# Performance work log

Hardware: AMD Instinct MI355X
Metric: run time of the kernel (lower is better)

The kernel has to match this reference:

```python
import jax, jax.numpy as jnp
import numpy as np
from jax import lax

VOCAB = 50000
EMB = 10
HID = 16


def setup_inputs() -> dict:
    key = jax.random.key(0)
    ks = jax.random.split(key, 8)
    B, T = 4096, 512
    x = jax.random.randint(ks[0], (B, T), 0, VOCAB + 1)
    emb = jax.random.normal(ks[1], (VOCAB + 1, EMB), dtype=jnp.float32)
    emb = emb.at[0].set(0.0)  # padding_idx=0 row is zeros
    s_ih = 1.0 / np.sqrt(HID)
    Wih = jax.random.uniform(ks[2], (4 * HID, EMB), minval=-s_ih, maxval=s_ih, dtype=jnp.float32)
    Whh = jax.random.uniform(ks[3], (4 * HID, HID), minval=-s_ih, maxval=s_ih, dtype=jnp.float32)
    bih = jax.random.uniform(ks[4], (4 * HID,), minval=-s_ih, maxval=s_ih, dtype=jnp.float32)
    bhh = jax.random.uniform(ks[5], (4 * HID,), minval=-s_ih, maxval=s_ih, dtype=jnp.float32)
    Wfc = jax.random.uniform(ks[6], (1, HID), minval=-s_ih, maxval=s_ih, dtype=jnp.float32)
    bfc = jax.random.uniform(ks[7], (1,), minval=-s_ih, maxval=s_ih, dtype=jnp.float32)
    return {"x": x, "emb": emb, "Wih": Wih, "Whh": Whh, "bih": bih, "bhh": bhh, "Wfc": Wfc, "bfc": bfc}


def _lstm_last_h(xe, Wih, Whh, bih, bhh):
    # xe: [B, T, EMB] -> final hidden state [B, HID]. PyTorch gate order: i, f, g, o.
    B = xe.shape[0]
    h0 = jnp.zeros((B, HID), dtype=xe.dtype)
    c0 = jnp.zeros((B, HID), dtype=xe.dtype)
    # Precompute input projections for all timesteps: [T, B, 4H]
    xproj = jnp.einsum('btе,ge->btg'.replace('\u0435', 'e'), xe, Wih) + bih + bhh
    xproj = xproj.transpose(1, 0, 2)

    def step(carry, xp_t):
        h, c = carry
        gates = xp_t + h @ Whh.T  # [B, 4H]
        i, f, g, o = jnp.split(gates, 4, axis=-1)
        i = jax.nn.sigmoid(i)
        f = jax.nn.sigmoid(f)
        g = jnp.tanh(g)
        o = jax.nn.sigmoid(o)
        c = f * c + i * g
        h = o * jnp.tanh(c)
        return (h, c), None

    (h, _), _ = lax.scan(step, (h0, c0), xproj)
    return h


def reference(x, emb, Wih, Whh, bih, bhh, Wfc, bfc):
    xe = emb[x]  # [B, T, EMB] embedding lookup (padding row 0 is zero)
    h = _lstm_last_h(xe, Wih, Whh, bih, bhh)  # [B, HID]
    out = h @ Wfc.T + bfc  # [B, 1]
    return jax.nn.sigmoid(out)
```

## Files before the change

kernel.cpp:

```cpp
#include <hip/hip_runtime.h>

#define T_LEN 512
#define NHID 16
#define NEMB 10
#define VOCAB1 50001
#define IROW 520

typedef float v2f __attribute__((ext_vector_type(2)));

__global__ __launch_bounds__(256) void build_table(
    const float* __restrict__ emb, const float* __restrict__ Wih,
    const float* __restrict__ bih, const float* __restrict__ bhh,
    float* __restrict__ tbl)
{
    const int tid = blockIdx.x * 256 + threadIdx.x;
    if (tid >= VOCAB1 * 16) return;
    const int v = tid >> 4, j = tid & 15;
    float e[NEMB];
    #pragma unroll
    for (int i = 0; i < NEMB; ++i) e[i] = emb[v * NEMB + i];
    float o[4];
    #pragma unroll
    for (int q = 0; q < 4; ++q) {
        const int r = q * 16 + j;
        float a = bih[r] + bhh[r];
        #pragma unroll
        for (int i = 0; i < NEMB; ++i) a += e[i] * Wih[r * NEMB + i];
        o[q] = a;
    }
    ((float4*)tbl)[tid] = make_float4(o[0], o[1], o[2], o[3]);
}

#define DPP_ROR(dst, src_i, r)                                                   \
    dst = __builtin_bit_cast(float, __builtin_amdgcn_update_dpp(                 \
              0, src_i, 0x120 + r, 0xF, 0xF, true))

__global__ __launch_bounds__(256) void lstm_dpp_kernel(
    const int*   __restrict__ x,
    const float* __restrict__ tbl,
    const float* __restrict__ Whh,
    const float* __restrict__ Wfc,
    const float* __restrict__ bfc,
    float*       __restrict__ out)
{
    __shared__ int idxs[16][IROW];

    const int tid = threadIdx.x;
    const int j   = tid & 15;
    const int lb  = tid >> 4;
    const int batch = blockIdx.x * 16 + lb;

    #pragma unroll 1
    for (int b = 0; b < 16; ++b) {
        const int* xr = x + (size_t)(blockIdx.x * 16 + b) * T_LEN;
        for (int t = tid; t < IROW; t += 256)
            idxs[b][t] = (t < T_LEN) ? (xr[t] << 4) : 0;
    }
    __syncthreads();

    float w[4][16];
    #pragma unroll
    for (int q = 0; q < 4; ++q) {
        const int row = (q * 16 + j) * NHID;
        #pragma unroll
        for (int r = 0; r < 16; ++r)
            w[q][r] = Whh[row + ((j - r) & 15)];
    }

    float h = 0.f, c = 0.f;
    const float NL2E  = -1.44269504088896f;
    const float NL2E2 = -2.88539008177793f;
    const float4* t4 = (const float4*)tbl;

    float4 pf[4];
    #pragma unroll
    for (int s = 0; s < 4; ++s)
        pf[s] = t4[idxs[lb][s] + j];

    #pragma unroll 1
    for (int t = 0; t < T_LEN; t += 4) {
        #pragma unroll
        for (int u = 0; u < 4; ++u) {
            const float4 tb = pf[u];
            pf[u] = t4[idxs[lb][t + 4 + u] + j];

            float hr[16];
            const int hvi = __builtin_bit_cast(int, h);
            hr[0] = h;
            DPP_ROR(hr[1],  hvi, 1);   DPP_ROR(hr[2],  hvi, 2);
            DPP_ROR(hr[3],  hvi, 3);   DPP_ROR(hr[4],  hvi, 4);
            DPP_ROR(hr[5],  hvi, 5);   DPP_ROR(hr[6],  hvi, 6);
            DPP_ROR(hr[7],  hvi, 7);   DPP_ROR(hr[8],  hvi, 8);
            DPP_ROR(hr[9],  hvi, 9);   DPP_ROR(hr[10], hvi, 10);
            DPP_ROR(hr[11], hvi, 11);  DPP_ROR(hr[12], hvi, 12);
            DPP_ROR(hr[13], hvi, 13);  DPP_ROR(hr[14], hvi, 14);
            DPP_ROR(hr[15], hvi, 15);

            float a0 = tb.x, a1 = tb.y, a2 = tb.z, a3 = tb.w;
            #pragma unroll
            for (int r = 0; r < 16; ++r) {
                a0 = fmaf(hr[r], w[0][r], a0);
                a1 = fmaf(hr[r], w[1][r], a1);
                a2 = fmaf(hr[r], w[2][r], a2);
                a3 = fmaf(hr[r], w[3][r], a3);
            }

            const float ig = __builtin_amdgcn_rcpf(1.f + __builtin_amdgcn_exp2f(a0 * NL2E));
            const float fg = __builtin_amdgcn_rcpf(1.f + __builtin_amdgcn_exp2f(a1 * NL2E));
            const float gg = 2.f * __builtin_amdgcn_rcpf(1.f + __builtin_amdgcn_exp2f(a2 * NL2E2)) - 1.f;
            const float og = __builtin_amdgcn_rcpf(1.f + __builtin_amdgcn_exp2f(a3 * NL2E));

            c = fg * c + ig * gg;
            const float tc = 2.f * __builtin_amdgcn_rcpf(1.f + __builtin_amdgcn_exp2f(c * NL2E2)) - 1.f;
            h = og * tc;
        }
    }

    float s = h * Wfc[j];
    s += __shfl_xor(s, 1, 64);
    s += __shfl_xor(s, 2, 64);
    s += __shfl_xor(s, 4, 64);
    s += __shfl_xor(s, 8, 64);
    if (j == 0)
        out[batch] = __builtin_amdgcn_rcpf(1.f + __builtin_amdgcn_exp2f((s + bfc[0]) * NL2E));
}

__global__ __launch_bounds__(256) void lstm_fb_kernel(
    const int*   __restrict__ x,
    const float* __restrict__ emb,
    const float* __restrict__ Wih,
    const float* __restrict__ Whh,
    const float* __restrict__ bih,
    const float* __restrict__ bhh,
    const float* __restrict__ Wfc,
    const float* __restrict__ bfc,
    float*       __restrict__ out)
{
    __shared__ int   idx_lds[T_LEN][17];
    __shared__ float hx[16][20];

    const int tid  = threadIdx.x;
    const int lane = tid & 63;
    const int j    = lane & 15;
    const int lb   = tid >> 4;
    const int batch = blockIdx.x * 16 + lb;

    for (int i = tid; i < 16 * T_LEN; i += 256) {
        const int b = i & 15;
        const int t = i >> 4;
        idx_lds[t][b] = x[(blockIdx.x * 16 + b) * T_LEN + t];
    }

    float wih[4][NEMB], bias[4];
    v2f w[4][8];
    #pragma unroll
    for (int q = 0; q < 4; ++q) {
        const int r = j + 16 * q;
        #pragma unroll
        for (int e = 0; e < NEMB; ++e) wih[q][e] = Wih[r * NEMB + e];
        #pragma unroll
        for (int p = 0; p < 8; ++p)
            w[q][p] = (v2f){Whh[r * NHID + 2 * p], Whh[r * NHID + 2 * p + 1]};
        bias[q] = bih[r] + bhh[r];
    }

    __syncthreads();

    v2f h2[8];
    #pragma unroll
    for (int p = 0; p < 8; ++p) h2[p] = (v2f){0.f, 0.f};
    float c = 0.f;

    const float NL2E  = -1.44269504088896f;
    const float NL2E2 = -2.88539008177793f;
    const float4* hp = (const float4*)&hx[lb][0];

    float2 xa, xb, xc, xd, xe2;
    {
        const float2* er = (const float2*)(emb + (long)idx_lds[0][lb] * NEMB);
        xa = er[0]; xb = er[1]; xc = er[2]; xd = er[3]; xe2 = er[4];
    }
    int idx_n = idx_lds[1][lb];

    #pragma unroll 1
    for (int t = 0; t < T_LEN; ++t) {
        const float xv[NEMB] = {xa.x, xa.y, xb.x, xb.y, xc.x, xc.y,
                                xd.x, xd.y, xe2.x, xe2.y};
        if (t + 1 < T_LEN) {
            const float2* er = (const float2*)(emb + (long)idx_n * NEMB);
            xa = er[0]; xb = er[1]; xc = er[2]; xd = er[3]; xe2 = er[4];
        }
        const int idx_nn = (t + 2 < T_LEN) ? idx_lds[t + 2][lb] : 0;

        float v[4];
        #pragma unroll
        for (int q = 0; q < 4; ++q) {
            float a = bias[q];
            #pragma unroll
            for (int e = 0; e < NEMB; ++e) a += xv[e] * wih[q][e];
            v[q] = a;
        }
        v2f a0 = (v2f){v[0], 0.f}, a1 = (v2f){v[1], 0.f};
        v2f a2 = (v2f){v[2], 0.f}, a3 = (v2f){v[3], 0.f};
        #pragma unroll
        for (int p = 0; p < 8; ++p) {
            a0 += h2[p] * w[0][p];
            a1 += h2[p] * w[1][p];
            a2 += h2[p] * w[2][p];
            a3 += h2[p] * w[3][p];
        }
        const float vi = a0.x + a0.y, vf = a1.x + a1.y;
        const float vg = a2.x + a2.y, vo = a3.x + a3.y;

        const float ig = __builtin_amdgcn_rcpf(1.f + __builtin_amdgcn_exp2f(vi * NL2E));
        const float fg = __builtin_amdgcn_rcpf(1.f + __builtin_amdgcn_exp2f(vf * NL2E));
        const float gg = 2.f * __builtin_amdgcn_rcpf(1.f + __builtin_amdgcn_exp2f(vg * NL2E2)) - 1.f;
        const float og = __builtin_amdgcn_rcpf(1.f + __builtin_amdgcn_exp2f(vo * NL2E));

        c = fg * c + ig * gg;
        const float tc = 2.f * __builtin_amdgcn_rcpf(1.f + __builtin_amdgcn_exp2f(c * NL2E2)) - 1.f;
        const float hv = og * tc;

        hx[lb][j] = hv;
        const float4 b0 = hp[0], b1 = hp[1], b2 = hp[2], b3 = hp[3];
        h2[0] = (v2f){b0.x, b0.y}; h2[1] = (v2f){b0.z, b0.w};
        h2[2] = (v2f){b1.x, b1.y}; h2[3] = (v2f){b1.z, b1.w};
        h2[4] = (v2f){b2.x, b2.y}; h2[5] = (v2f){b2.z, b2.w};
        h2[6] = (v2f){b3.x, b3.y}; h2[7] = (v2f){b3.z, b3.w};

        idx_n = idx_nn;
    }

    if (j == 0) {
        float logit = bfc[0];
        #pragma unroll
        for (int p = 0; p < 8; ++p)
            logit += h2[p].x * Wfc[2 * p] + h2[p].y * Wfc[2 * p + 1];
        out[batch] = __builtin_amdgcn_rcpf(1.f + __builtin_amdgcn_exp2f(logit * NL2E));
    }
}

extern "C" void kernel_launch(void* const* d_in, const int* in_sizes, int n_in,
                              void* d_out, int out_size, void* d_ws, size_t ws_size,
                              hipStream_t stream) {
    const int*   x   = (const int*)  d_in[0];
    const float* emb = (const float*)d_in[1];
    const float* Wih = (const float*)d_in[2];
    const float* Whh = (const float*)d_in[3];
    const float* bih = (const float*)d_in[4];
    const float* bhh = (const float*)d_in[5];
    const float* Wfc = (const float*)d_in[6];
    const float* bfc = (const float*)d_in[7];
    float* outp = (float*)d_out;

    const int B = in_sizes[0] / T_LEN;
    const size_t TABLE_BYTES = (size_t)VOCAB1 * 64 * sizeof(float);

    if (ws_size >= TABLE_BYTES) {
        float* tbl = (float*)d_ws;
        build_table<<<(VOCAB1 * 16 + 255) / 256, 256, 0, stream>>>(emb, Wih, bih, bhh, tbl);
        lstm_dpp_kernel<<<B / 16, 256, 0, stream>>>(x, tbl, Whh, Wfc, bfc, outp);
    } else {
        lstm_fb_kernel<<<B / 16, 256, 0, stream>>>(x, emb, Wih, Whh, bih, bhh, Wfc, bfc, outp);
    }
}
```

Measured before the change: 180.1 us.

## Split LSTM recurrent matvec across two half-waves and combine via swizzle

Each batch row now uses 32 lanes instead of 16. Each half-group of 16 lanes computes 8 of the 16 recurrent dot-product terms, and the two partial sums are combined with a ds_swizzle lane exchange. This halves the serial DPP/FMA chain per timestep and doubles the grid, giving more waves per CU to hide latency. Embedding-table indices are also prefetched from LDS one iteration ahead. In exchange it adds an LDS-based swizzle and an extra DPP plus select on the critical path of every step.

```diff
diff --git a/kernel.cpp b/kernel.cpp
--- a/kernel.cpp
+++ b/kernel.cpp
@@ -4,7 +4,7 @@
 #define NHID 16
 #define NEMB 10
 #define VOCAB1 50001
-#define IROW 520
+#define IROW 521
 
 typedef float v2f __attribute__((ext_vector_type(2)));
 
@@ -35,7 +35,7 @@
     dst = __builtin_bit_cast(float, __builtin_amdgcn_update_dpp(                 \
               0, src_i, 0x120 + r, 0xF, 0xF, true))
 
-__global__ __launch_bounds__(256) void lstm_dpp_kernel(
+__global__ __launch_bounds__(256) void lstm_ks_kernel(
     const int*   __restrict__ x,
     const float* __restrict__ tbl,
     const float* __restrict__ Whh,
@@ -43,28 +43,29 @@
     const float* __restrict__ bfc,
     float*       __restrict__ out)
 {
-    __shared__ int idxs[16][IROW];
+    __shared__ int idxs[8][IROW];
 
     const int tid = threadIdx.x;
     const int j   = tid & 15;
-    const int lb  = tid >> 4;
-    const int batch = blockIdx.x * 16 + lb;
+    const int hi  = (tid >> 4) & 1;
+    const int lb  = tid >> 5;
+    const int batch = blockIdx.x * 8 + lb;
 
     #pragma unroll 1
-    for (int b = 0; b < 16; ++b) {
-        const int* xr = x + (size_t)(blockIdx.x * 16 + b) * T_LEN;
+    for (int b = 0; b < 8; ++b) {
+        const int* xr = x + (size_t)(blockIdx.x * 8 + b) * T_LEN;
         for (int t = tid; t < IROW; t += 256)
             idxs[b][t] = (t < T_LEN) ? (xr[t] << 4) : 0;
     }
     __syncthreads();
 
-    float w[4][16];
+    float w[4][8];
     #pragma unroll
     for (int q = 0; q < 4; ++q) {
         const int row = (q * 16 + j) * NHID;
         #pragma unroll
-        for (int r = 0; r < 16; ++r)
-            w[q][r] = Whh[row + ((j - r) & 15)];
+        for (int s = 0; s < 8; ++s)
+            w[q][s] = Whh[row + ((j - hi * 8 - s) & 15)];
     }
 
     float h = 0.f, c = 0.f;
@@ -73,37 +74,58 @@
     const float4* t4 = (const float4*)tbl;
 
     float4 pf[4];
-    #pragma unroll
-    for (int s = 0; s < 4; ++s)
+    int iv[4];
+    #pragma unroll
+    for (int s = 0; s < 4; ++s) {
         pf[s] = t4[idxs[lb][s] + j];
+        iv[s] = idxs[lb][4 + s];
+    }
 
     #pragma unroll 1
     for (int t = 0; t < T_LEN; t += 4) {
+        int ivn[4];
+        #pragma unroll
+        for (int u = 0; u < 4; ++u) ivn[u] = idxs[lb][t + 8 + u];
+
         #pragma unroll
         for (int u = 0; u < 4; ++u) {
             const float4 tb = pf[u];
-            pf[u] = t4[idxs[lb][t + 4 + u] + j];
-
-            float hr[16];
+            pf[u] = t4[iv[u] + j];
+
             const int hvi = __builtin_bit_cast(int, h);
-            hr[0] = h;
-            DPP_ROR(hr[1],  hvi, 1);   DPP_ROR(hr[2],  hvi, 2);
-            DPP_ROR(hr[3],  hvi, 3);   DPP_ROR(hr[4],  hvi, 4);
-            DPP_ROR(hr[5],  hvi, 5);   DPP_ROR(hr[6],  hvi, 6);
-            DPP_ROR(hr[7],  hvi, 7);   DPP_ROR(hr[8],  hvi, 8);
-            DPP_ROR(hr[9],  hvi, 9);   DPP_ROR(hr[10], hvi, 10);
-            DPP_ROR(hr[11], hvi, 11);  DPP_ROR(hr[12], hvi, 12);
-            DPP_ROR(hr[13], hvi, 13);  DPP_ROR(hr[14], hvi, 14);
-            DPP_ROR(hr[15], hvi, 15);
-
-            float a0 = tb.x, a1 = tb.y, a2 = tb.z, a3 = tb.w;
+            float h8; DPP_ROR(h8, hvi, 8);
+            const float hsrc = hi ? h8 : h;
+            const int hsi = __builtin_bit_cast(int, hsrc);
+
+            float hr[8];
+            hr[0] = hsrc;
+            DPP_ROR(hr[1], hsi, 1);  DPP_ROR(hr[2], hsi, 2);
+            DPP_ROR(hr[3], hsi, 3);  DPP_ROR(hr[4], hsi, 4);
+            DPP_ROR(hr[5], hsi, 5);  DPP_ROR(hr[6], hsi, 6);
+            DPP_ROR(hr[7], hsi, 7);
+
+            float p0 = 0.f, p1 = 0.f, p2 = 0.f, p3 = 0.f;
             #pragma unroll
-            for (int r = 0; r < 16; ++r) {
-                a0 = fmaf(hr[r], w[0][r], a0);
-                a1 = fmaf(hr[r], w[1][r], a1);
-                a2 = fmaf(hr[r], w[2][r], a2);
-                a3 = fmaf(hr[r], w[3][r], a3);
+            for (int s = 0; s < 8; ++s) {
+                p0 = fmaf(hr[s], w[0][s], p0);
+                p1 = fmaf(hr[s], w[1][s], p1);
+                p2 = fmaf(hr[s], w[2][s], p2);
+                p3 = fmaf(hr[s], w[3][s], p3);
             }
+
+            const float q0 = __builtin_bit_cast(float,
+                __builtin_amdgcn_ds_swizzle(__builtin_bit_cast(int, p0), 0x401F));
+            const float q1 = __builtin_bit_cast(float,
+                __builtin_amdgcn_ds_swizzle(__builtin_bit_cast(int, p1), 0x401F));
+            const float q2 = __builtin_bit_cast(float,
+                __builtin_amdgcn_ds_swizzle(__builtin_bit_cast(int, p2), 0x401F));
+            const float q3 = __builtin_bit_cast(float,
+                __builtin_amdgcn_ds_swizzle(__builtin_bit_cast(int, p3), 0x401F));
+
+            const float a0 = tb.x + (p0 + q0);
+            const float a1 = tb.y + (p1 + q1);
+            const float a2 = tb.z + (p2 + q2);
+            const float a3 = tb.w + (p3 + q3);
 
             const float ig = __builtin_amdgcn_rcpf(1.f + __builtin_amdgcn_exp2f(a0 * NL2E));
             const float fg = __builtin_amdgcn_rcpf(1.f + __builtin_amdgcn_exp2f(a1 * NL2E));
@@ -114,6 +136,9 @@
             const float tc = 2.f * __builtin_amdgcn_rcpf(1.f + __builtin_amdgcn_exp2f(c * NL2E2)) - 1.f;
             h = og * tc;
         }
+
+        #pragma unroll
+        for (int u = 0; u < 4; ++u) iv[u] = ivn[u];
     }
 
     float s = h * Wfc[j];
@@ -121,7 +146,7 @@
     s += __shfl_xor(s, 2, 64);
     s += __shfl_xor(s, 4, 64);
     s += __shfl_xor(s, 8, 64);
-    if (j == 0)
+    if ((tid & 31) == 0)
         out[batch] = __builtin_amdgcn_rcpf(1.f + __builtin_amdgcn_exp2f((s + bfc[0]) * NL2E));
 }
 
@@ -259,7 +284,7 @@
     if (ws_size >= TABLE_BYTES) {
         float* tbl = (float*)d_ws;
         build_table<<<(VOCAB1 * 16 + 255) / 256, 256, 0, stream>>>(emb, Wih, bih, bhh, tbl);
-        lstm_dpp_kernel<<<B / 16, 256, 0, stream>>>(x, tbl, Whh, Wfc, bfc, outp);
+        lstm_ks_kernel<<<B / 8, 256, 0, stream>>>(x, tbl, Whh, Wfc, bfc, outp);
     } else {
         lstm_fb_kernel<<<B / 16, 256, 0, stream>>>(x, emb, Wih, Whh, bih, bhh, Wfc, bfc, outp);
     }
```

New measurement: 205.2 us. 1.14x slower.
